# Performance work log

Measured on AMD Instinct MI355X. Metric: run time of the kernel, lower is better.

The kernel has to match this reference:

```python
import jax, jax.numpy as jnp
import numpy as np

C = 64

def setup_inputs() -> dict:
    key = jax.random.key(0)
    ks = jax.random.split(key, 4)
    B, H, W = 16, 256, 256
    feature = jax.random.normal(ks[0], (B, C, H, W), dtype=jnp.float32)
    confidence = jax.random.uniform(ks[1], (B, 1, H, W), dtype=jnp.float32)
    # input_proj: Conv1d(C, C, k=1) -> weight squeezed to [C, C]; state_proj likewise
    Wi = jax.random.normal(ks[2], (C, C), dtype=jnp.float32) * 0.05
    bi = jnp.zeros((C,), dtype=jnp.float32)
    Ws = jax.random.normal(ks[3], (C, C), dtype=jnp.float32) * 0.05
    bs = jnp.zeros((C,), dtype=jnp.float32)
    bias = jnp.zeros((C,), dtype=jnp.float32)
    return {"feature": feature, "confidence": confidence, "Wi": Wi, "bi": bi,
            "Ws": Ws, "bs": bs, "bias": bias}


def reference(feature, confidence, Wi, bi, Ws, bs, bias):
    # direction = 'lr' (propagate left-to-right along width)
    B, Cc, H, W = feature.shape
    # [B,C,H,W] -> [B*H, C, W]  (independent rows)
    seq = feature.transpose(0, 2, 1, 3).reshape(B * H, Cc, W)
    gate = confidence.transpose(0, 2, 1, 3).reshape(B * H, 1, W)
    # pointwise input projection (Conv1d k=1)
    proj = jnp.einsum('oc,ncw->now', Wi, seq) + bi[None, :, None]
    xs = (jnp.moveaxis(proj, -1, 0), jnp.moveaxis(gate, -1, 0))  # [W,N,C], [W,N,1]

    def step(prev, x):
        p_t, g_t = x                      # [N,C], [N,1]
        rec = (prev * g_t) @ Ws.T + bs    # state_proj on gated previous state
        cur = jax.nn.relu(p_t + rec + bias)
        return cur, cur

    init = jnp.zeros((B * H, Cc), dtype=feature.dtype)
    _, ys = jax.lax.scan(step, init, xs)  # [W, N, C]
    out = jnp.moveaxis(ys, 0, -1).reshape(B, H, Cc, W).transpose(0, 2, 1, 3)
    return out
```

## Files before the change

kernel.cpp:

```cpp
#include <hip/hip_runtime.h>
#include <hip/hip_bf16.h>


typedef __attribute__((ext_vector_type(8))) short short8;
typedef __attribute__((ext_vector_type(4))) short short4v;
typedef __attribute__((ext_vector_type(2))) short short2v;
typedef __attribute__((ext_vector_type(4))) float f32x4;

union FragU { unsigned int u[4]; short8 v; };
union PkU { unsigned int u; short2v s2; };

__device__ __forceinline__ unsigned int pk2(float a, float b) {
    unsigned short lo = __bfloat16_as_ushort(__float2bfloat16(a));
    unsigned short hi = __bfloat16_as_ushort(__float2bfloat16(b));
    return (unsigned int)lo | ((unsigned int)hi << 16);
}
__device__ __forceinline__ float b2f(short x) {
    return __uint_as_float(((unsigned int)(unsigned short)x) << 16);
}

__device__ __forceinline__ int fsi(int w, int n, int c) {
    return (w * 1024 + n * 64 + c) ^ ((n & 7) << 3);
}
__device__ __forceinline__ int sti(int n, int c) {
    return (n * 64 + c) ^ ((n & 7) << 3);
}
__device__ __forceinline__ int ogi(int o, int n, int w) {
    return (o * 256 + n * 16 + w) ^ ((((o >> 2) ^ (n >> 2)) & 3) << 2);
}

template<int V> struct Ic { static constexpr int value = V; };

__global__ __launch_bounds__(256) void dp_fused_kernel(
    const float* __restrict__ feat, const float* __restrict__ conf,
    const float* __restrict__ Wi, const float* __restrict__ bi,
    const float* __restrict__ Ws, const float* __restrict__ bs,
    const float* __restrict__ bias, float* __restrict__ outp)
{
    __shared__ unsigned short fs[2][16384];
    __shared__ unsigned short st[2][1024];
    __shared__ unsigned short og[16384];

    const int tid = threadIdx.x;
    const int lane = tid & 63;
    const int t = tid >> 6;
    const int l15 = lane & 15, g4 = lane >> 4;
    const int nb = blockIdx.x;
    const int b = nb >> 4, h0 = (nb & 15) * 16;

    FragU Ai[2], As[2];
    #pragma unroll
    for (int hh = 0; hh < 2; ++hh) {
        const float* si = Wi + (16 * t + l15) * 64 + 32 * hh + g4 * 8;
        const float* ss = Ws + (16 * t + l15) * 64 + 32 * hh + g4 * 8;
        #pragma unroll
        for (int d = 0; d < 4; ++d) {
            Ai[hh].u[d] = pk2(si[2 * d], si[2 * d + 1]);
            As[hh].u[d] = pk2(ss[2 * d], ss[2 * d + 1]);
        }
    }
    float binit[4];
    #pragma unroll
    for (int r = 0; r < 4; ++r) {
        int o = 16 * t + 4 * g4 + r;
        binit[r] = bi[o] + bs[o] + bias[o];
    }

    const float* fb = feat + (size_t)b * 64 * 65536 + (size_t)h0 * 256;
    const float* gb = conf + ((size_t)(b * 256) + h0 + l15) * 256;

    f32x4 fst[2][2][4];
    auto issue_feat = [&](int w0) {
        #pragma unroll
        for (int k = 0; k < 2; ++k) {
            int p = tid + 256 * k; int cp = p >> 4; int n = p & 15;
            const float* base = fb + (size_t)(2 * cp) * 65536 + n * 256 + w0;
            #pragma unroll
            for (int row = 0; row < 2; ++row)
                #pragma unroll
                for (int j = 0; j < 4; ++j)
                    fst[k][row][j] = *(const f32x4*)(base + row * 65536 + j * 4);
        }
    };
    auto write_fs = [&](int buf) {
        #pragma unroll
        for (int k = 0; k < 2; ++k) {
            int p = tid + 256 * k; int cp = p >> 4; int n = p & 15;
            #pragma unroll
            for (int j = 0; j < 4; ++j)
                #pragma unroll
                for (int e = 0; e < 4; ++e) {
                    PkU pk; pk.u = pk2(fst[k][0][j][e], fst[k][1][j][e]);
                    *(short2v*)&fs[buf][fsi(j * 4 + e, n, 2 * cp)] = pk.s2;
                }
        }
    };
    auto dump = [&](int wprev) {
        const int n = lane >> 2, wq = lane & 3;
        #pragma unroll
        for (int k = 0; k < 16; ++k) {
            const int o = 16 * t + k;
            short4v d = *(const short4v*)&og[ogi(o, n, wq * 4)];
            f32x4 o4 = { b2f(d.x), b2f(d.y), b2f(d.z), b2f(d.w) };
            *(f32x4*)(outp + ((size_t)(b * 64 + o) * 256 + h0 + n) * 256 + wprev + wq * 4) = o4;
        }
    };

    f32x4 gqA[4], gqB[4]; float glA, glB;

    issue_feat(0);
    #pragma unroll
    for (int q = 0; q < 4; ++q) gqA[q] = *(const f32x4*)(gb + q * 4);
    glA = gb[16];
    { short4v z = {0, 0, 0, 0}; *(short4v*)&st[0][tid * 4] = z; }
    write_fs(0);
    __syncthreads();

    auto run_chunk = [&](auto pc, int cc) {
        constexpr int P = decltype(pc)::value;
        f32x4 (&gqc)[4] = P ? gqB : gqA;
        f32x4 (&gqn)[4] = P ? gqA : gqB;
        float &glc = P ? glB : glA;
        float &gln = P ? glA : glB;
        const int w0 = cc * 16;
        float curE[4];
        #pragma unroll
        for (int u = 0; u < 16; ++u) {
            if (u == 0 && cc > 0) dump(w0 - 16);

            short8 F0 = *(const short8*)&fs[P][fsi(u, l15, g4 * 8)];
            short8 F1 = *(const short8*)&fs[P][fsi(u, l15, 32 + g4 * 8)];
            short8 S0 = *(const short8*)&st[u & 1][sti(l15, g4 * 8)];
            short8 S1 = *(const short8*)&st[u & 1][sti(l15, 32 + g4 * 8)];
            f32x4 acc = { binit[0], binit[1], binit[2], binit[3] };
            acc = __builtin_amdgcn_mfma_f32_16x16x32_bf16(Ai[0].v, F0, acc, 0, 0, 0);
            acc = __builtin_amdgcn_mfma_f32_16x16x32_bf16(Ai[1].v, F1, acc, 0, 0, 0);
            acc = __builtin_amdgcn_mfma_f32_16x16x32_bf16(As[0].v, S0, acc, 0, 0, 0);
            acc = __builtin_amdgcn_mfma_f32_16x16x32_bf16(As[1].v, S1, acc, 0, 0, 0);
            float cur0 = fmaxf(acc[0], 0.f), cur1 = fmaxf(acc[1], 0.f);
            float cur2 = fmaxf(acc[2], 0.f), cur3 = fmaxf(acc[3], 0.f);

            if (u == 0 && cc < 15) issue_feat(w0 + 16);
            if (u == 2 && cc < 15) {
                #pragma unroll
                for (int q = 0; q < 4; ++q)
                    gqn[q] = *(const f32x4*)(gb + w0 + 16 + q * 4);
                int gi = w0 + 32; if (gi > 255) gi = 255;
                gln = gb[gi];
            }

            if ((u & 1) == 0) {
                curE[0] = cur0; curE[1] = cur1; curE[2] = cur2; curE[3] = cur3;
            } else {
                const float cc4[4] = { cur0, cur1, cur2, cur3 };
                #pragma unroll
                for (int r = 0; r < 4; ++r) {
                    PkU pk; pk.u = pk2(curE[r], cc4[r]);
                    *(short2v*)&og[ogi(16 * t + 4 * g4 + r, l15, u - 1)] = pk.s2;
                }
            }

            if (u == 14 && cc < 15) write_fs(P ^ 1);

            if (!(cc == 15 && u == 15)) {
                float gv = (u < 15) ? gqc[(u + 1) >> 2][(u + 1) & 3] : glc;
                PkU a, c;
                a.u = pk2(cur0 * gv, cur1 * gv);
                c.u = pk2(cur2 * gv, cur3 * gv);
                short4v sv = { a.s2.x, a.s2.y, c.s2.x, c.s2.y };
                *(short4v*)&st[(u + 1) & 1][sti(l15, 16 * t + 4 * g4)] = sv;
            }
            __syncthreads();
        }
    };

    #pragma unroll 1
    for (int c2 = 0; c2 < 8; ++c2) {
        run_chunk(Ic<0>{}, c2 * 2);
        run_chunk(Ic<1>{}, c2 * 2 + 1);
    }
    dump(240);
}

extern "C" void kernel_launch(void* const* d_in, const int* in_sizes, int n_in,
                              void* d_out, int out_size, void* d_ws, size_t ws_size,
                              hipStream_t stream) {
    const float* feat = (const float*)d_in[0];
    const float* conf = (const float*)d_in[1];
    const float* Wi   = (const float*)d_in[2];
    const float* bi   = (const float*)d_in[3];
    const float* Ws   = (const float*)d_in[4];
    const float* bs   = (const float*)d_in[5];
    const float* bias = (const float*)d_in[6];
    float* out = (float*)d_out;
    (void)d_ws; (void)ws_size; (void)in_sizes; (void)n_in; (void)out_size;

    dp_fused_kernel<<<256, 256, 0, stream>>>(feat, conf, Wi, bi, Ws, bs, bias, out);
}
```

Before: 193.4 us.

## Prefetch next feature fragment, split MFMA chains, spread loads and dumps, lighter barrier

```diff
diff --git a/kernel.cpp b/kernel.cpp
--- a/kernel.cpp
+++ b/kernel.cpp
@@ -28,6 +28,8 @@
 __device__ __forceinline__ int ogi(int o, int n, int w) {
     return (o * 256 + n * 16 + w) ^ ((((o >> 2) ^ (n >> 2)) & 3) << 2);
 }
+
+#define BAR() asm volatile("s_waitcnt lgkmcnt(0)\n\ts_barrier" ::: "memory")
 
 template<int V> struct Ic { static constexpr int value = V; };
 
@@ -70,17 +72,13 @@
     const float* gb = conf + ((size_t)(b * 256) + h0 + l15) * 256;
 
     f32x4 fst[2][2][4];
-    auto issue_feat = [&](int w0) {
-        #pragma unroll
-        for (int k = 0; k < 2; ++k) {
-            int p = tid + 256 * k; int cp = p >> 4; int n = p & 15;
-            const float* base = fb + (size_t)(2 * cp) * 65536 + n * 256 + w0;
-            #pragma unroll
-            for (int row = 0; row < 2; ++row)
-                #pragma unroll
-                for (int j = 0; j < 4; ++j)
-                    fst[k][row][j] = *(const f32x4*)(base + row * 65536 + j * 4);
-        }
+    auto load_part = [&](auto kc, auto rc, int w0n) {
+        constexpr int K = decltype(kc)::value, R = decltype(rc)::value;
+        const int p = tid + 256 * K; const int cp = p >> 4; const int n = p & 15;
+        const float* base = fb + (size_t)(2 * cp + R) * 65536 + n * 256 + w0n;
+        #pragma unroll
+        for (int j = 0; j < 4; ++j)
+            fst[K][R][j] = *(const f32x4*)(base + j * 4);
     };
     auto write_fs = [&](int buf) {
         #pragma unroll
@@ -95,10 +93,11 @@
                 }
         }
     };
-    auto dump = [&](int wprev) {
+    auto dump_half = [&](auto hc, int wprev) {
+        constexpr int H = decltype(hc)::value;
         const int n = lane >> 2, wq = lane & 3;
         #pragma unroll
-        for (int k = 0; k < 16; ++k) {
+        for (int k = 8 * H; k < 8 * H + 8; ++k) {
             const int o = 16 * t + k;
             short4v d = *(const short4v*)&og[ogi(o, n, wq * 4)];
             f32x4 o4 = { b2f(d.x), b2f(d.y), b2f(d.z), b2f(d.w) };
@@ -107,14 +106,18 @@
     };
 
     f32x4 gqA[4], gqB[4]; float glA, glB;
-
-    issue_feat(0);
+    short8 Fp[2][2];
+
+    load_part(Ic<0>{}, Ic<0>{}, 0); load_part(Ic<0>{}, Ic<1>{}, 0);
+    load_part(Ic<1>{}, Ic<0>{}, 0); load_part(Ic<1>{}, Ic<1>{}, 0);
     #pragma unroll
     for (int q = 0; q < 4; ++q) gqA[q] = *(const f32x4*)(gb + q * 4);
     glA = gb[16];
     { short4v z = {0, 0, 0, 0}; *(short4v*)&st[0][tid * 4] = z; }
     write_fs(0);
-    __syncthreads();
+    BAR();
+    Fp[0][0] = *(const short8*)&fs[0][fsi(0, l15, g4 * 8)];
+    Fp[0][1] = *(const short8*)&fs[0][fsi(0, l15, 32 + g4 * 8)];
 
     auto run_chunk = [&](auto pc, int cc) {
         constexpr int P = decltype(pc)::value;
@@ -126,28 +129,40 @@
         float curE[4];
         #pragma unroll
         for (int u = 0; u < 16; ++u) {
-            if (u == 0 && cc > 0) dump(w0 - 16);
-
-            short8 F0 = *(const short8*)&fs[P][fsi(u, l15, g4 * 8)];
-            short8 F1 = *(const short8*)&fs[P][fsi(u, l15, 32 + g4 * 8)];
             short8 S0 = *(const short8*)&st[u & 1][sti(l15, g4 * 8)];
             short8 S1 = *(const short8*)&st[u & 1][sti(l15, 32 + g4 * 8)];
-            f32x4 acc = { binit[0], binit[1], binit[2], binit[3] };
-            acc = __builtin_amdgcn_mfma_f32_16x16x32_bf16(Ai[0].v, F0, acc, 0, 0, 0);
-            acc = __builtin_amdgcn_mfma_f32_16x16x32_bf16(Ai[1].v, F1, acc, 0, 0, 0);
-            acc = __builtin_amdgcn_mfma_f32_16x16x32_bf16(As[0].v, S0, acc, 0, 0, 0);
-            acc = __builtin_amdgcn_mfma_f32_16x16x32_bf16(As[1].v, S1, acc, 0, 0, 0);
-            float cur0 = fmaxf(acc[0], 0.f), cur1 = fmaxf(acc[1], 0.f);
-            float cur2 = fmaxf(acc[2], 0.f), cur3 = fmaxf(acc[3], 0.f);
-
-            if (u == 0 && cc < 15) issue_feat(w0 + 16);
-            if (u == 2 && cc < 15) {
-                #pragma unroll
-                for (int q = 0; q < 4; ++q)
-                    gqn[q] = *(const f32x4*)(gb + w0 + 16 + q * 4);
-                int gi = w0 + 32; if (gi > 255) gi = 255;
-                gln = gb[gi];
-            }
+            {
+                const unsigned short* fsrc = (u < 15) ? fs[P] : fs[P ^ 1];
+                const int wn = (u < 15) ? u + 1 : 0;
+                Fp[(u + 1) & 1][0] = *(const short8*)&fsrc[fsi(wn, l15, g4 * 8)];
+                Fp[(u + 1) & 1][1] = *(const short8*)&fsrc[fsi(wn, l15, 32 + g4 * 8)];
+            }
+            if (u == 0 && cc > 0) dump_half(Ic<0>{}, w0 - 16);
+            if (u == 1 && cc > 0) dump_half(Ic<1>{}, w0 - 16);
+            if (cc < 15) {
+                if (u == 0) load_part(Ic<0>{}, Ic<0>{}, w0 + 16);
+                if (u == 1) load_part(Ic<0>{}, Ic<1>{}, w0 + 16);
+                if (u == 2) load_part(Ic<1>{}, Ic<0>{}, w0 + 16);
+                if (u == 3) load_part(Ic<1>{}, Ic<1>{}, w0 + 16);
+                if (u == 2) {
+                    #pragma unroll
+                    for (int q = 0; q < 4; ++q)
+                        gqn[q] = *(const f32x4*)(gb + w0 + 16 + q * 4);
+                    int gi = w0 + 32; if (gi > 255) gi = 255;
+                    gln = gb[gi];
+                }
+            }
+
+            f32x4 accA = { binit[0], binit[1], binit[2], binit[3] };
+            f32x4 accB = { 0.f, 0.f, 0.f, 0.f };
+            accA = __builtin_amdgcn_mfma_f32_16x16x32_bf16(Ai[0].v, Fp[u & 1][0], accA, 0, 0, 0);
+            accB = __builtin_amdgcn_mfma_f32_16x16x32_bf16(Ai[1].v, Fp[u & 1][1], accB, 0, 0, 0);
+            accA = __builtin_amdgcn_mfma_f32_16x16x32_bf16(As[0].v, S0, accA, 0, 0, 0);
+            accB = __builtin_amdgcn_mfma_f32_16x16x32_bf16(As[1].v, S1, accB, 0, 0, 0);
+            float cur0 = fmaxf(accA[0] + accB[0], 0.f);
+            float cur1 = fmaxf(accA[1] + accB[1], 0.f);
+            float cur2 = fmaxf(accA[2] + accB[2], 0.f);
+            float cur3 = fmaxf(accA[3] + accB[3], 0.f);
 
             if ((u & 1) == 0) {
                 curE[0] = cur0; curE[1] = cur1; curE[2] = cur2; curE[3] = cur3;
@@ -170,16 +185,17 @@
                 short4v sv = { a.s2.x, a.s2.y, c.s2.x, c.s2.y };
                 *(short4v*)&st[(u + 1) & 1][sti(l15, 16 * t + 4 * g4)] = sv;
             }
-            __syncthreads();
+            BAR();
         }
     };
 
     #pragma unroll 1
     for (int c2 = 0; c2 < 8; ++c2) {
-        run_chunk(Ic<0>{}, c2 * 2);
-        run_chunk(Ic<1>{}, c2 * 2 + 1);
+        run_chunk(Ic<0>{}, 2 * c2);
+        run_chunk(Ic<1>{}, 2 * c2 + 1);
     }
-    dump(240);
+    dump_half(Ic<0>{}, 240);
+    dump_half(Ic<1>{}, 240);
 }
 
 extern "C" void kernel_launch(void* const* d_in, const int* in_sizes, int n_in,
```

Measured after the change: 196.8 us. No clear change (+1.8%).

## Warp-specialize recurrence: one compute wave, loader waves, store wave

Applied to the files above, without the earlier changes.

```diff
diff --git a/kernel.cpp b/kernel.cpp
--- a/kernel.cpp
+++ b/kernel.cpp
@@ -22,164 +22,207 @@
 __device__ __forceinline__ int fsi(int w, int n, int c) {
     return (w * 1024 + n * 64 + c) ^ ((n & 7) << 3);
 }
-__device__ __forceinline__ int sti(int n, int c) {
-    return (n * 64 + c) ^ ((n & 7) << 3);
-}
 __device__ __forceinline__ int ogi(int o, int n, int w) {
     return (o * 256 + n * 16 + w) ^ ((((o >> 2) ^ (n >> 2)) & 3) << 2);
 }
 
+#define BAR() asm volatile("s_waitcnt lgkmcnt(0)\n\ts_barrier" ::: "memory")
+
 template<int V> struct Ic { static constexpr int value = V; };
 
-__global__ __launch_bounds__(256) void dp_fused_kernel(
+__global__ __launch_bounds__(256, 1) void dp_v5_kernel(
     const float* __restrict__ feat, const float* __restrict__ conf,
     const float* __restrict__ Wi, const float* __restrict__ bi,
     const float* __restrict__ Ws, const float* __restrict__ bs,
     const float* __restrict__ bias, float* __restrict__ outp)
 {
     __shared__ unsigned short fs[2][16384];
-    __shared__ unsigned short st[2][1024];
-    __shared__ unsigned short og[16384];
+    __shared__ unsigned short og[2][16384];
 
     const int tid = threadIdx.x;
     const int lane = tid & 63;
-    const int t = tid >> 6;
+    const int wid = tid >> 6;
     const int l15 = lane & 15, g4 = lane >> 4;
     const int nb = blockIdx.x;
     const int b = nb >> 4, h0 = (nb & 15) * 16;
 
-    FragU Ai[2], As[2];
-    #pragma unroll
-    for (int hh = 0; hh < 2; ++hh) {
-        const float* si = Wi + (16 * t + l15) * 64 + 32 * hh + g4 * 8;
-        const float* ss = Ws + (16 * t + l15) * 64 + 32 * hh + g4 * 8;
-        #pragma unroll
-        for (int d = 0; d < 4; ++d) {
-            Ai[hh].u[d] = pk2(si[2 * d], si[2 * d + 1]);
-            As[hh].u[d] = pk2(ss[2 * d], ss[2 * d + 1]);
+    const float* fb = feat + (size_t)b * 64 * 65536 + (size_t)h0 * 256;
+
+    if (wid == 0) {
+        const float* gb = conf + ((size_t)(b * 256) + h0 + l15) * 256;
+
+        FragU Ai[4][2], As[4][2];
+        #pragma unroll
+        for (int t = 0; t < 4; ++t)
+            #pragma unroll
+            for (int h = 0; h < 2; ++h) {
+                const float* si = Wi + (16 * t + l15) * 64 + 32 * h + g4 * 8;
+                const float* ss = Ws + (16 * t + l15) * 64;
+                #pragma unroll
+                for (int d = 0; d < 4; ++d) {
+                    Ai[t][h].u[d] = pk2(si[2 * d], si[2 * d + 1]);
+                    const int c0 = 16 * (2 * h + (d >> 1)) + 4 * g4 + 2 * (d & 1);
+                    As[t][h].u[d] = pk2(ss[c0], ss[c0 + 1]);
+                }
+            }
+        f32x4 binit[4];
+        #pragma unroll
+        for (int t = 0; t < 4; ++t)
+            #pragma unroll
+            for (int r = 0; r < 4; ++r) {
+                int o = 16 * t + 4 * g4 + r;
+                binit[t][r] = bi[o] + bs[o] + bias[o];
+            }
+
+        f32x4 gqA[4], gqB[4];
+        #pragma unroll
+        for (int q = 0; q < 4; ++q) gqA[q] = *(const f32x4*)(gb + 4 * q);
+
+        FragU S0, S1;
+        #pragma unroll
+        for (int d = 0; d < 4; ++d) { S0.u[d] = 0u; S1.u[d] = 0u; }
+
+        float curE[4][4];
+
+        BAR();
+
+        auto run_chunk = [&](auto pc, int cc) {
+            constexpr int P = decltype(pc)::value;
+            f32x4 (&gqc)[4] = P ? gqB : gqA;
+            f32x4 (&gqn)[4] = P ? gqA : gqB;
+            const int w0 = cc * 16;
+            #pragma unroll
+            for (int u = 0; u < 16; ++u) {
+                short8 F0 = *(const short8*)&fs[P][fsi(u, l15, 8 * g4)];
+                short8 F1 = *(const short8*)&fs[P][fsi(u, l15, 32 + 8 * g4)];
+
+                if (u == 2 && cc < 15) {
+                    #pragma unroll
+                    for (int q = 0; q < 4; ++q)
+                        gqn[q] = *(const f32x4*)(gb + w0 + 16 + 4 * q);
+                }
+
+                f32x4 a0 = binit[0], a1 = binit[1], a2 = binit[2], a3 = binit[3];
+                a0 = __builtin_amdgcn_mfma_f32_16x16x32_bf16(Ai[0][0].v, F0, a0, 0, 0, 0);
+                a1 = __builtin_amdgcn_mfma_f32_16x16x32_bf16(Ai[1][0].v, F0, a1, 0, 0, 0);
+                a2 = __builtin_amdgcn_mfma_f32_16x16x32_bf16(Ai[2][0].v, F0, a2, 0, 0, 0);
+                a3 = __builtin_amdgcn_mfma_f32_16x16x32_bf16(Ai[3][0].v, F0, a3, 0, 0, 0);
+                a0 = __builtin_amdgcn_mfma_f32_16x16x32_bf16(Ai[0][1].v, F1, a0, 0, 0, 0);
+                a1 = __builtin_amdgcn_mfma_f32_16x16x32_bf16(Ai[1][1].v, F1, a1, 0, 0, 0);
+                a2 = __builtin_amdgcn_mfma_f32_16x16x32_bf16(Ai[2][1].v, F1, a2, 0, 0, 0);
+                a3 = __builtin_amdgcn_mfma_f32_16x16x32_bf16(Ai[3][1].v, F1, a3, 0, 0, 0);
+                a0 = __builtin_amdgcn_mfma_f32_16x16x32_bf16(As[0][0].v, S0.v, a0, 0, 0, 0);
+                a1 = __builtin_amdgcn_mfma_f32_16x16x32_bf16(As[1][0].v, S0.v, a1, 0, 0, 0);
+                a2 = __builtin_amdgcn_mfma_f32_16x16x32_bf16(As[2][0].v, S0.v, a2, 0, 0, 0);
+                a3 = __builtin_amdgcn_mfma_f32_16x16x32_bf16(As[3][0].v, S0.v, a3, 0, 0, 0);
+                a0 = __builtin_amdgcn_mfma_f32_16x16x32_bf16(As[0][1].v, S1.v, a0, 0, 0, 0);
+                a1 = __builtin_amdgcn_mfma_f32_16x16x32_bf16(As[1][1].v, S1.v, a1, 0, 0, 0);
+                a2 = __builtin_amdgcn_mfma_f32_16x16x32_bf16(As[2][1].v, S1.v, a2, 0, 0, 0);
+                a3 = __builtin_amdgcn_mfma_f32_16x16x32_bf16(As[3][1].v, S1.v, a3, 0, 0, 0);
+
+                float cur[4][4];
+                #pragma unroll
+                for (int r = 0; r < 4; ++r) {
+                    cur[0][r] = fmaxf(a0[r], 0.f);
+                    cur[1][r] = fmaxf(a1[r], 0.f);
+                    cur[2][r] = fmaxf(a2[r], 0.f);
+                    cur[3][r] = fmaxf(a3[r], 0.f);
+                }
+
+                if ((u & 1) == 0) {
+                    #pragma unroll
+                    for (int t = 0; t < 4; ++t)
+                        #pragma unroll
+                        for (int r = 0; r < 4; ++r) curE[t][r] = cur[t][r];
+                } else {
+                    #pragma unroll
+                    for (int t = 0; t < 4; ++t)
+                        #pragma unroll
+                        for (int r = 0; r < 4; ++r) {
+                            PkU pk; pk.u = pk2(curE[t][r], cur[t][r]);
+                            *(short2v*)&og[P][ogi(16 * t + 4 * g4 + r, l15, u - 1)] = pk.s2;
+                        }
+                }
+
+                if (!(cc == 15 && u == 15)) {
+                    float gv = (u < 15) ? gqc[(u + 1) >> 2][(u + 1) & 3] : gqn[0][0];
+                    float g0[4], g1[4], g2[4], g3[4];
+                    #pragma unroll
+                    for (int r = 0; r < 4; ++r) {
+                        g0[r] = cur[0][r] * gv; g1[r] = cur[1][r] * gv;
+                        g2[r] = cur[2][r] * gv; g3[r] = cur[3][r] * gv;
+                    }
+                    S0.u[0] = pk2(g0[0], g0[1]); S0.u[1] = pk2(g0[2], g0[3]);
+                    S0.u[2] = pk2(g1[0], g1[1]); S0.u[3] = pk2(g1[2], g1[3]);
+                    S1.u[0] = pk2(g2[0], g2[1]); S1.u[1] = pk2(g2[2], g2[3]);
+                    S1.u[2] = pk2(g3[0], g3[1]); S1.u[3] = pk2(g3[2], g3[3]);
+                }
+            }
+            BAR();
+        };
+
+        #pragma unroll 1
+        for (int c2 = 0; c2 < 8; ++c2) {
+            run_chunk(Ic<0>{}, 2 * c2);
+            run_chunk(Ic<1>{}, 2 * c2 + 1);
         }
+    } else if (wid <= 2) {
+        const int cb2 = (wid - 1) * 16;
+        const int n = lane & 15;
+
+        auto stage = [&](int buf, int w0) {
+            f32x4 ra[4][2][4];
+            #pragma unroll
+            for (int pi = 0; pi < 4; ++pi) {
+                const int cp = cb2 + 4 * pi + g4;
+                const float* p0 = fb + (size_t)(2 * cp) * 65536 + n * 256 + w0;
+                #pragma unroll
+                for (int row = 0; row < 2; ++row)
+                    #pragma unroll
+                    for (int q = 0; q < 4; ++q)
+                        ra[pi][row][q] = *(const f32x4*)(p0 + row * 65536 + 4 * q);
+            }
+            #pragma unroll
+            for (int pi = 0; pi < 4; ++pi) {
+                const int cp = cb2 + 4 * pi + g4;
+                #pragma unroll
+                for (int q = 0; q < 4; ++q)
+                    #pragma unroll
+                    for (int e = 0; e < 4; ++e) {
+                        PkU pk; pk.u = pk2(ra[pi][0][q][e], ra[pi][1][q][e]);
+                        *(short2v*)&fs[buf][fsi(4 * q + e, n, 2 * cp)] = pk.s2;
+                    }
+            }
+        };
+
+        stage(0, 0);
+        BAR();
+        #pragma unroll 1
+        for (int cc = 0; cc < 16; ++cc) {
+            if (cc < 15) stage((cc + 1) & 1, (cc + 1) * 16);
+            BAR();
+        }
+    } else {
+        const int n = (lane >> 2) & 15, wq = lane & 3;
+        float* const ob = outp + ((size_t)(b * 64) * 256 + h0 + n) * 256 + 4 * wq;
+
+        auto drain = [&](int buf, int wpr) {
+            #pragma unroll 8
+            for (int o = 0; o < 64; ++o) {
+                short4v d = *(const short4v*)&og[buf][ogi(o, n, 4 * wq)];
+                f32x4 o4 = { b2f(d.x), b2f(d.y), b2f(d.z), b2f(d.w) };
+                *(f32x4*)(ob + (size_t)o * 65536 + wpr) = o4;
+            }
+        };
+
+        BAR();
+        #pragma unroll 1
+        for (int cc = 0; cc < 16; ++cc) {
+            if (cc > 0) drain((cc - 1) & 1, (cc - 1) * 16);
+            BAR();
+        }
+        drain(1, 240);
     }
-    float binit[4];
-    #pragma unroll
-    for (int r = 0; r < 4; ++r) {
-        int o = 16 * t + 4 * g4 + r;
-        binit[r] = bi[o] + bs[o] + bias[o];
-    }
-
-    const float* fb = feat + (size_t)b * 64 * 65536 + (size_t)h0 * 256;
-    const float* gb = conf + ((size_t)(b * 256) + h0 + l15) * 256;
-
-    f32x4 fst[2][2][4];
-    auto issue_feat = [&](int w0) {
-        #pragma unroll
-        for (int k = 0; k < 2; ++k) {
-            int p = tid + 256 * k; int cp = p >> 4; int n = p & 15;
-            const float* base = fb + (size_t)(2 * cp) * 65536 + n * 256 + w0;
-            #pragma unroll
-            for (int row = 0; row < 2; ++row)
-                #pragma unroll
-                for (int j = 0; j < 4; ++j)
-                    fst[k][row][j] = *(const f32x4*)(base + row * 65536 + j * 4);
-        }
-    };
-    auto write_fs = [&](int buf) {
-        #pragma unroll
-        for (int k = 0; k < 2; ++k) {
-            int p = tid + 256 * k; int cp = p >> 4; int n = p & 15;
-            #pragma unroll
-            for (int j = 0; j < 4; ++j)
-                #pragma unroll
-                for (int e = 0; e < 4; ++e) {
-                    PkU pk; pk.u = pk2(fst[k][0][j][e], fst[k][1][j][e]);
-                    *(short2v*)&fs[buf][fsi(j * 4 + e, n, 2 * cp)] = pk.s2;
-                }
-        }
-    };
-    auto dump = [&](int wprev) {
-        const int n = lane >> 2, wq = lane & 3;
-        #pragma unroll
-        for (int k = 0; k < 16; ++k) {
-            const int o = 16 * t + k;
-            short4v d = *(const short4v*)&og[ogi(o, n, wq * 4)];
-            f32x4 o4 = { b2f(d.x), b2f(d.y), b2f(d.z), b2f(d.w) };
-            *(f32x4*)(outp + ((size_t)(b * 64 + o) * 256 + h0 + n) * 256 + wprev + wq * 4) = o4;
-        }
-    };
-
-    f32x4 gqA[4], gqB[4]; float glA, glB;
-
-    issue_feat(0);
-    #pragma unroll
-    for (int q = 0; q < 4; ++q) gqA[q] = *(const f32x4*)(gb + q * 4);
-    glA = gb[16];
-    { short4v z = {0, 0, 0, 0}; *(short4v*)&st[0][tid * 4] = z; }
-    write_fs(0);
-    __syncthreads();
-
-    auto run_chunk = [&](auto pc, int cc) {
-        constexpr int P = decltype(pc)::value;
-        f32x4 (&gqc)[4] = P ? gqB : gqA;
-        f32x4 (&gqn)[4] = P ? gqA : gqB;
-        float &glc = P ? glB : glA;
-        float &gln = P ? glA : glB;
-        const int w0 = cc * 16;
-        float curE[4];
-        #pragma unroll
-        for (int u = 0; u < 16; ++u) {
-            if (u == 0 && cc > 0) dump(w0 - 16);
-
-            short8 F0 = *(const short8*)&fs[P][fsi(u, l15, g4 * 8)];
-            short8 F1 = *(const short8*)&fs[P][fsi(u, l15, 32 + g4 * 8)];
-            short8 S0 = *(const short8*)&st[u & 1][sti(l15, g4 * 8)];
-            short8 S1 = *(const short8*)&st[u & 1][sti(l15, 32 + g4 * 8)];
-            f32x4 acc = { binit[0], binit[1], binit[2], binit[3] };
-            acc = __builtin_amdgcn_mfma_f32_16x16x32_bf16(Ai[0].v, F0, acc, 0, 0, 0);
-            acc = __builtin_amdgcn_mfma_f32_16x16x32_bf16(Ai[1].v, F1, acc, 0, 0, 0);
-            acc = __builtin_amdgcn_mfma_f32_16x16x32_bf16(As[0].v, S0, acc, 0, 0, 0);
-            acc = __builtin_amdgcn_mfma_f32_16x16x32_bf16(As[1].v, S1, acc, 0, 0, 0);
-            float cur0 = fmaxf(acc[0], 0.f), cur1 = fmaxf(acc[1], 0.f);
-            float cur2 = fmaxf(acc[2], 0.f), cur3 = fmaxf(acc[3], 0.f);
-
-            if (u == 0 && cc < 15) issue_feat(w0 + 16);
-            if (u == 2 && cc < 15) {
-                #pragma unroll
-                for (int q = 0; q < 4; ++q)
-                    gqn[q] = *(const f32x4*)(gb + w0 + 16 + q * 4);
-                int gi = w0 + 32; if (gi > 255) gi = 255;
-                gln = gb[gi];
-            }
-
-            if ((u & 1) == 0) {
-                curE[0] = cur0; curE[1] = cur1; curE[2] = cur2; curE[3] = cur3;
-            } else {
-                const float cc4[4] = { cur0, cur1, cur2, cur3 };
-                #pragma unroll
-                for (int r = 0; r < 4; ++r) {
-                    PkU pk; pk.u = pk2(curE[r], cc4[r]);
-                    *(short2v*)&og[ogi(16 * t + 4 * g4 + r, l15, u - 1)] = pk.s2;
-                }
-            }
-
-            if (u == 14 && cc < 15) write_fs(P ^ 1);
-
-            if (!(cc == 15 && u == 15)) {
-                float gv = (u < 15) ? gqc[(u + 1) >> 2][(u + 1) & 3] : glc;
-                PkU a, c;
-                a.u = pk2(cur0 * gv, cur1 * gv);
-                c.u = pk2(cur2 * gv, cur3 * gv);
-                short4v sv = { a.s2.x, a.s2.y, c.s2.x, c.s2.y };
-                *(short4v*)&st[(u + 1) & 1][sti(l15, 16 * t + 4 * g4)] = sv;
-            }
-            __syncthreads();
-        }
-    };
-
-    #pragma unroll 1
-    for (int c2 = 0; c2 < 8; ++c2) {
-        run_chunk(Ic<0>{}, c2 * 2);
-        run_chunk(Ic<1>{}, c2 * 2 + 1);
-    }
-    dump(240);
 }
 
 extern "C" void kernel_launch(void* const* d_in, const int* in_sizes, int n_in,
@@ -195,5 +238,5 @@
     float* out = (float*)d_out;
     (void)d_ws; (void)ws_size; (void)in_sizes; (void)n_in; (void)out_size;
 
-    dp_fused_kernel<<<256, 256, 0, stream>>>(feat, conf, Wi, bi, Ws, bs, bias, out);
-}
+    dp_v5_kernel<<<256, 256, 0, stream>>>(feat, conf, Wi, bi, Ws, bs, bias, out);
+}
```

Measured after the change: 184.3 us. 1.05x faster.
